# Kernel optimization log

Hardware: AMD Instinct MI355X
Metric: run time of the kernel (lower is better)

## Reference

```python
import jax, jax.numpy as jnp
import numpy as np

B, L0, L1, NS, D, H, NL, HM = 16, 512, 256, 32, 256, 8, 4, 4
T = L0 + L1 + NS + 1
HD = D // H
EPS = 1e-5
SCALE = HD ** -0.5


def setup_inputs() -> dict:
    key = jax.random.key(0)
    ks = jax.random.split(key, 20)
    s = 0.02
    return {
        'seq_tokens_0': jax.random.normal(ks[0], (B, L0, D), jnp.float32),
        'seq_tokens_1': jax.random.normal(ks[1], (B, L1, D), jnp.float32),
        'seq_lens_0': jax.random.randint(ks[2], (B,), 0, L0),
        'seq_lens_1': jax.random.randint(ks[3], (B,), 0, L1),
        'ns_tokens': jax.random.normal(ks[4], (B, NS, D), jnp.float32),
        'domain_emb': jax.random.normal(ks[5], (2, D), jnp.float32) * s,
        'cls_token': jax.random.normal(ks[6], (1, 1, D), jnp.float32) * s,
        'ln1_w': jnp.ones((NL, D), jnp.float32),
        'ln1_b': jnp.zeros((NL, D), jnp.float32),
        'qkv_w': jax.random.normal(ks[7], (NL, D, 3 * D), jnp.float32) * s,
        'qkv_b': jnp.zeros((NL, 3 * D), jnp.float32),
        'out_w': jax.random.normal(ks[8], (NL, D, D), jnp.float32) * s,
        'out_b': jnp.zeros((NL, D), jnp.float32),
        'ln2_w': jnp.ones((NL, D), jnp.float32),
        'ln2_b': jnp.zeros((NL, D), jnp.float32),
        'ffn1_w': jax.random.normal(ks[9], (NL, D, HM * D), jnp.float32) * s,
        'ffn1_b': jnp.zeros((NL, HM * D), jnp.float32),
        'ffn2_w': jax.random.normal(ks[10], (NL, HM * D, D), jnp.float32) * s,
        'ffn2_b': jnp.zeros((NL, D), jnp.float32),
        'fln_w': jnp.ones((D,), jnp.float32),
        'fln_b': jnp.zeros((D,), jnp.float32),
    }


def _ln(x, w, b):
    m = jnp.mean(x, -1, keepdims=True)
    v = jnp.var(x, -1, keepdims=True)
    return (x - m) * jax.lax.rsqrt(v + EPS) * w + b


def _build_mask(seq_lens_0, seq_lens_1):
    # static block structure: intra-domain causal, S<->NS bidirectional, CLS sink row
    base = jnp.zeros((T, T), bool)
    base = base.at[:L0, :L0].set(jnp.tril(jnp.ones((L0, L0), bool)))
    base = base.at[L0:L0 + L1, L0:L0 + L1].set(jnp.tril(jnp.ones((L1, L1), bool)))
    ns_s, ns_e = L0 + L1, L0 + L1 + NS
    base = base.at[:ns_s, ns_s:ns_e].set(True)   # S -> NS
    base = base.at[ns_s:ns_e, :ns_e].set(True)   # NS -> S and NS -> NS
    base = base.at[T - 1, :ns_e].set(True)       # CLS reads all S/NS
    base = base.at[T - 1, T - 1].set(True)       # CLS reads itself
    # per-batch padding mask on keys of each seq segment
    kv = jnp.ones((B, T), bool)
    kv = kv.at[:, :L0].set(jnp.arange(L0)[None, :] < seq_lens_0[:, None])
    kv = kv.at[:, L0:L0 + L1].set(jnp.arange(L1)[None, :] < seq_lens_1[:, None])
    return base[None] & kv[:, None, :]  # [B, T, T]


def _attention(x, mask, qkv_w, qkv_b, out_w, out_b):
    qkv = (x @ qkv_w + qkv_b).reshape(B, T, 3, H, HD)
    q, k, v = qkv[:, :, 0], qkv[:, :, 1], qkv[:, :, 2]
    scores = jnp.einsum('bqhd,bkhd->bhqk', q, k) * SCALE
    m = mask[:, None]  # [B,1,T,T]
    s = jnp.where(m, scores, -jnp.inf)
    any_valid = jnp.any(m, -1, keepdims=True)
    mx = jnp.where(any_valid, jnp.max(s, -1, keepdims=True), 0.0)
    e = jnp.exp(s - mx)  # masked entries exp(-inf)=0
    denom = jnp.sum(e, -1, keepdims=True)
    probs = e / jnp.maximum(denom, 1e-30)  # fully-masked rows -> zeros
    out = jnp.einsum('bhqk,bkhd->bqhd', probs, v).reshape(B, T, D)
    return out @ out_w + out_b


def reference(seq_tokens_0, seq_tokens_1, seq_lens_0, seq_lens_1, ns_tokens,
              domain_emb, cls_token, ln1_w, ln1_b, qkv_w, qkv_b, out_w, out_b,
              ln2_w, ln2_b, ffn1_w, ffn1_b, ffn2_w, ffn2_b, fln_w, fln_b):
    t0 = seq_tokens_0 + domain_emb[0][None, None, :]
    t1 = seq_tokens_1 + domain_emb[1][None, None, :]
    cls = jnp.broadcast_to(cls_token, (B, 1, D))
    x = jnp.concatenate([t0, t1, ns_tokens, cls], axis=1)  # [B,T,D]
    mask = _build_mask(seq_lens_0, seq_lens_1)
    for l in range(NL):
        x = x + _attention(_ln(x, ln1_w[l], ln1_b[l]), mask,
                           qkv_w[l], qkv_b[l], out_w[l], out_b[l])
        h = _ln(x, ln2_w[l], ln2_b[l])
        h = jax.nn.gelu(h @ ffn1_w[l] + ffn1_b[l], approximate=False)
        x = x + h @ ffn2_w[l] + ffn2_b[l]
    x = _ln(x, fln_w, fln_b)
    return x[:, -1, :]  # CLS state [B,D]
```

## Files before the change

kernel.cpp:

```cpp
#include <hip/hip_runtime.h>
#include <hip/hip_bf16.h>
#include <math.h>

typedef __attribute__((ext_vector_type(8))) unsigned short ushort8;
typedef __attribute__((ext_vector_type(8))) short short8;
typedef __attribute__((ext_vector_type(4))) float f32x4;
typedef __attribute__((ext_vector_type(4))) unsigned short ushort4v;
typedef __attribute__((ext_vector_type(4))) int i32x4;
typedef unsigned int u32;

namespace {
constexpr int B = 16, L0 = 512, L1 = 256, NS = 32, D = 256, H = 8, NL = 4, HM = 4;
constexpr int T = L0 + L1 + NS + 1;
constexpr int HD = D / H;
constexpr int NTOK = B * T;
constexpr int NS_S = L0 + L1;
constexpr int NS_E = NS_S + NS;
constexpr int TPAD = 832;
constexpr float EPS = 1e-5f;
constexpr float SCALE = 0.17677669529663687f;
constexpr float SCL2  = 0.17677669529663687f * 1.4426950408889634f;
}

__device__ __forceinline__ ushort f2bf(float f) {
    union { float f; unsigned u; } v; v.f = f;
    return (ushort)((v.u + 0x7fffu + ((v.u >> 16) & 1u)) >> 16);
}

__device__ __forceinline__ u32 cvtpk(float a, float b) {
    u32 r;
    asm("v_cvt_pk_bf16_f32 %0, %1, %2" : "=v"(r) : "v"(a), "v"(b));
    return r;
}

__device__ __forceinline__ void gload_lds16(const void* g, void* l) {
    __builtin_amdgcn_global_load_lds(
        (const __attribute__((address_space(1))) u32*)g,
        (__attribute__((address_space(3))) u32*)l, 16, 0, 0);
}

__global__ __launch_bounds__(256) void k_build_x(
    const float* __restrict__ s0, const float* __restrict__ s1,
    const float* __restrict__ ns, const float* __restrict__ dom,
    const float* __restrict__ cls, float* __restrict__ x)
{
    const int row = blockIdx.x;
    const int b = row / T, t = row % T;
    const int d = threadIdx.x;
    float v;
    if (t < L0)        v = s0[((size_t)b * L0 + t) * D + d] + dom[d];
    else if (t < NS_S) v = s1[((size_t)b * L1 + (t - L0)) * D + d] + dom[D + d];
    else if (t < NS_E) v = ns[((size_t)b * NS + (t - NS_S)) * D + d];
    else               v = cls[d];
    x[(size_t)row * D + d] = v;
}

__global__ __launch_bounds__(256) void k_wprep(
    const float* __restrict__ src, ushort* __restrict__ dst, int K, int N)
{
    const size_t off = (size_t)blockIdx.z * K * N;
    src += off; dst += off;
    __shared__ float t[32][33];
    const int kb = blockIdx.x * 32, nb = blockIdx.y * 32;
    const int c = threadIdx.x & 31, r8 = threadIdx.x >> 5;
#pragma unroll
    for (int rr = 0; rr < 32; rr += 8)
        t[r8 + rr][c] = src[(size_t)(kb + r8 + rr) * N + nb + c];
    __syncthreads();
#pragma unroll
    for (int rr = 0; rr < 32; rr += 8)
        dst[(size_t)(nb + r8 + rr) * K + kb + c] = f2bf(t[c][r8 + rr]);
}

__global__ __launch_bounds__(256) void k_ln(
    const float* __restrict__ x, const float* __restrict__ w,
    const float* __restrict__ bsh, ushort* __restrict__ y, int nrows)
{
    const int wid = threadIdx.x >> 6, lane = threadIdx.x & 63;
    const int row = blockIdx.x * 4 + wid;
    if (row >= nrows) return;
    float4 v = *(const float4*)(x + (size_t)row * D + lane * 4);
    float s  = v.x + v.y + v.z + v.w;
    float ss = v.x * v.x + v.y * v.y + v.z * v.z + v.w * v.w;
#pragma unroll
    for (int o = 32; o; o >>= 1) { s += __shfl_xor(s, o); ss += __shfl_xor(ss, o); }
    const float mean = s * (1.f / D);
    const float var  = ss * (1.f / D) - mean * mean;
    const float r = rsqrtf(var + EPS);
    float4 wv = *(const float4*)(w + lane * 4);
    float4 bv = *(const float4*)(bsh + lane * 4);
    ushort4v o4;
    o4[0] = f2bf((v.x - mean) * r * wv.x + bv.x);
    o4[1] = f2bf((v.y - mean) * r * wv.y + bv.y);
    o4[2] = f2bf((v.z - mean) * r * wv.z + bv.z);
    o4[3] = f2bf((v.w - mean) * r * wv.w + bv.w);
    *(ushort4v*)(y + (size_t)row * D + lane * 4) = o4;
}

__global__ __launch_bounds__(64) void k_final_ln(
    const float* __restrict__ x, const float* __restrict__ w,
    const float* __restrict__ bsh, float* __restrict__ out)
{
    const int b = blockIdx.x, lane = threadIdx.x;
    const float* xr = x + (size_t)(b * T + (T - 1)) * D;
    float4 v = *(const float4*)(xr + lane * 4);
    float s  = v.x + v.y + v.z + v.w;
    float ss = v.x * v.x + v.y * v.y + v.z * v.z + v.w * v.w;
#pragma unroll
    for (int o = 32; o; o >>= 1) { s += __shfl_xor(s, o); ss += __shfl_xor(ss, o); }
    const float mean = s * (1.f / D);
    const float var  = ss * (1.f / D) - mean * mean;
    const float r = rsqrtf(var + EPS);
    float4 wv = *(const float4*)(w + lane * 4);
    float4 bv = *(const float4*)(bsh + lane * 4);
    float4 o4;
    o4.x = (v.x - mean) * r * wv.x + bv.x;
    o4.y = (v.y - mean) * r * wv.y + bv.y;
    o4.z = (v.z - mean) * r * wv.z + bv.z;
    o4.w = (v.w - mean) * r * wv.w + bv.w;
    *(float4*)(out + (size_t)b * D + lane * 4) = o4;
}

template<bool GELU, bool RES, bool OBF>
__global__ __launch_bounds__(256) void k_gemm_mfma(
    const ushort* __restrict__ A, const ushort* __restrict__ Wt,
    const float* __restrict__ bias, void* __restrict__ Cout,
    const float* __restrict__ res, int M, int N, int K)
{
    __shared__ ushort As[2][128 * 64];
    __shared__ ushort Bs[2][128 * 64];
    const int tid = threadIdx.x;
    const int lane = tid & 63, w = tid >> 6;
    const int lo = lane & 15, g = lane >> 4;
    const int wr = w >> 1, wc = w & 1;
    const int m0 = blockIdx.x * 128, n0 = blockIdx.y * 128;

    f32x4 zero = {0.f, 0.f, 0.f, 0.f};
    f32x4 acc[4][4];
#pragma unroll
    for (int mi = 0; mi < 4; ++mi)
#pragma unroll
        for (int ni = 0; ni < 4; ++ni) acc[mi][ni] = zero;

    const ushort* srcA[4];
    const ushort* srcB[4];
    int ldsOff[4];
#pragma unroll
    for (int i = 0; i < 4; ++i) {
        const int idx16 = (w * 4 + i) * 64 + lane;
        const int row = idx16 >> 3;
        const int scb = ((idx16 & 7) * 16) ^ ((row & 7) << 4);
        int arow = m0 + row; if (arow >= M) arow = M - 1;
        srcA[i] = A  + (size_t)arow * K + (scb >> 1);
        srcB[i] = Wt + (size_t)(n0 + row) * K + (scb >> 1);
        ldsOff[i] = (w * 4 + i) * 512;
    }

    const int NT = K >> 6;

#pragma unroll
    for (int i = 0; i < 4; ++i) {
        gload_lds16(srcA[i], &As[0][ldsOff[i]]);
        gload_lds16(srcB[i], &Bs[0][ldsOff[i]]);
    }
    asm volatile("s_waitcnt vmcnt(0)");
    __syncthreads();

    for (int t = 0; t < NT; ++t) {
        const int buf = t & 1;
        if (t + 1 < NT) {
            const int nb = buf ^ 1, ko = (t + 1) * 64;
#pragma unroll
            for (int i = 0; i < 4; ++i) {
                gload_lds16(srcA[i] + ko, &As[nb][ldsOff[i]]);
                gload_lds16(srcB[i] + ko, &Bs[nb][ldsOff[i]]);
            }
        }
#pragma unroll
        for (int kk = 0; kk < 2; ++kk) {
            const int kb = (kk * 64 + g * 16) ^ ((lo & 7) << 4);
            short8 af[4], bfr[4];
#pragma unroll
            for (int mi = 0; mi < 4; ++mi) {
                const int r = wr * 64 + mi * 16 + lo;
                af[mi] = *(const short8*)&As[buf][r * 64 + (kb >> 1)];
            }
#pragma unroll
            for (int ni = 0; ni < 4; ++ni) {
                const int r = wc * 64 + ni * 16 + lo;
                bfr[ni] = *(const short8*)&Bs[buf][r * 64 + (kb >> 1)];
            }
#pragma unroll
            for (int mi = 0; mi < 4; ++mi)
#pragma unroll
                for (int ni = 0; ni < 4; ++ni)
                    acc[mi][ni] = __builtin_amdgcn_mfma_f32_16x16x32_bf16(
                        af[mi], bfr[ni], acc[mi][ni], 0, 0, 0);
        }
        asm volatile("s_waitcnt vmcnt(0)");
        __syncthreads();
    }

    float bv[4];
#pragma unroll
    for (int ni = 0; ni < 4; ++ni) bv[ni] = bias[n0 + wc * 64 + ni * 16 + lo];
#pragma unroll
    for (int mi = 0; mi < 4; ++mi) {
#pragma unroll
        for (int i = 0; i < 4; ++i) {
            const int row = m0 + wr * 64 + mi * 16 + g * 4 + i;
            if (row < M) {
#pragma unroll
                for (int ni = 0; ni < 4; ++ni) {
                    const int col = n0 + wc * 64 + ni * 16 + lo;
                    float v = acc[mi][ni][i] + bv[ni];
                    if (GELU) v = 0.5f * v * (1.0f + erff(v * 0.70710678118654752f));
                    if (RES)  v += res[(size_t)row * N + col];
                    if (OBF) ((ushort*)Cout)[(size_t)row * N + col] = f2bf(v);
                    else     ((float*)Cout)[(size_t)row * N + col] = v;
                }
            }
        }
    }
}

__global__ __launch_bounds__(256) void k_repack(
    const ushort* __restrict__ qkv, ushort* __restrict__ Kb, ushort* __restrict__ Vt)
{
    const int bh = blockIdx.x, tt = blockIdx.y;
    const int b = bh >> 3, h = bh & 7;
    const int tid = threadIdx.x;
    const int r = tid >> 2, c = tid & 3;
    const int t = tt * 64 + r;
    __shared__ ushort vtile[64][40];
    ushort8 k8 = {0,0,0,0,0,0,0,0}, v8 = {0,0,0,0,0,0,0,0};
    if (t < T) {
        const ushort* kp = qkv + ((size_t)(b * T + t) * 3 + 1) * D + h * HD + c * 8;
        k8 = *(const ushort8*)kp;
        v8 = *(const ushort8*)(kp + D);
    }
    *(ushort8*)(Kb + ((size_t)bh * TPAD + tt * 64 + r) * HD + c * 8) = k8;
    *(ushort8*)&vtile[r][c * 8] = v8;
    __syncthreads();
    const int d = tid >> 3, cc = tid & 7;
    ushort8 o;
#pragma unroll
    for (int j = 0; j < 8; ++j) o[j] = vtile[cc * 8 + j][d];
    *(ushort8*)(Vt + ((size_t)bh * HD + d) * TPAD + tt * 64 + cc * 8) = o;
}

__global__ __launch_bounds__(256) void k_flash(
    const ushort* __restrict__ qkv, const ushort* __restrict__ Kb,
    const ushort* __restrict__ Vt, const int* __restrict__ len0,
    const int* __restrict__ len1, ushort* __restrict__ out)
{
    const int bh = blockIdx.x;
    const int qt = 12 - blockIdx.y;
    const int b = bh >> 3, h = bh & 7;
    const int tid = threadIdx.x, lane = tid & 63, w = tid >> 6;
    const int lo = lane & 15, g = lane >> 4;
    const int b4 = g & 1, b5 = g >> 1;
    const int q = qt * 64 + w * 16 + lo;
    const int l0b = len0[b], lim01 = L0 + len1[b];

    int klo = 0, klim;
    if (q < L0)        klim = q;
    else if (q < NS_S) { klo = L0; klim = q; }
    else if (q < NS_E) klim = NS_E - 1;
    else               klim = q;

    int qrow = q; if (qrow > T - 1) qrow = T - 1;
    short8 qf = *(const short8*)(qkv + ((size_t)(b * T + qrow) * 3) * D + h * HD + g * 8);

    const ushort* Kbase = Kb + (size_t)bh * TPAD * HD;
    const ushort* Vbase = Vt + (size_t)bh * HD * TPAD;

    f32x4 acc0 = {0.f, 0.f, 0.f, 0.f}, acc1 = {0.f, 0.f, 0.f, 0.f};
    float mrow = -1e30f, srow = 0.f;

    const int kts = (qt >= 8 && qt < 12) ? 8 : 0;
    const int ntiles = (qt < 12) ? (qt - kts + 2) : 13;
    auto ktile = [&](int it) { int kt = kts + it; return kt > qt ? 12 : kt; };

    short8 kf[4];
    {
        const int k0 = ktile(0) * 64;
#pragma unroll
        for (int n = 0; n < 4; ++n)
            kf[n] = *(const short8*)(Kbase + (size_t)(k0 + n * 16 + lo) * HD + g * 8);
    }

    for (int it = 0; it < ntiles; ++it) {
        const int k0 = ktile(it) * 64;

        const ushort* V0 = Vbase + k0;
        short8 a00 = *(const short8*)(V0 + (size_t)lo * TPAD + g * 8);
        short8 a01 = *(const short8*)(V0 + (size_t)lo * TPAD + 32 + g * 8);
        short8 a10 = *(const short8*)(V0 + (size_t)(16 + lo) * TPAD + g * 8);
        short8 a11 = *(const short8*)(V0 + (size_t)(16 + lo) * TPAD + 32 + g * 8);

        float pv[4][4];
        float tmax = -1e30f;
#pragma unroll
        for (int n = 0; n < 4; ++n) {
            f32x4 z = {0.f, 0.f, 0.f, 0.f};
            f32x4 sn = __builtin_amdgcn_mfma_f32_16x16x32_bf16(kf[n], qf, z, 0, 0, 0);
#pragma unroll
            for (int i = 0; i < 4; ++i) {
                const int k = k0 + n * 16 + g * 4 + i;
                const bool inNS = (k >= NS_S) & (k < NS_E);
                const bool kval = (k < l0b) | ((k >= L0) & (k < lim01)) | (k >= NS_S);
                const bool m = ((k >= klo) & (k <= klim) & kval) | inNS;
                const float sv = m ? sn[i] * SCL2 : -1e30f;
                pv[n][i] = sv;
                tmax = fmaxf(tmax, sv);
            }
        }

        short8 kf2[4];
        if (it + 1 < ntiles) {
            const int k1 = ktile(it + 1) * 64;
#pragma unroll
            for (int n = 0; n < 4; ++n)
                kf2[n] = *(const short8*)(Kbase + (size_t)(k1 + n * 16 + lo) * HD + g * 8);
        }

        tmax = fmaxf(tmax, __shfl_xor(tmax, 16));
        tmax = fmaxf(tmax, __shfl_xor(tmax, 32));
        const float mnew = fmaxf(mrow, tmax);
        const float scl = exp2f(mrow - mnew);
        mrow = mnew;

        u32 C0[4], C1[4];
        float psum = 0.f;
#pragma unroll
        for (int n = 0; n < 4; ++n) {
            float e0 = exp2f(pv[n][0] - mnew);
            float e1 = exp2f(pv[n][1] - mnew);
            float e2 = exp2f(pv[n][2] - mnew);
            float e3 = exp2f(pv[n][3] - mnew);
            psum += (e0 + e1) + (e2 + e3);
            C0[n] = cvtpk(e0, e1);
            C1[n] = cvtpk(e2, e3);
        }
        psum += __shfl_xor(psum, 16);
        psum += __shfl_xor(psum, 32);
        srow = srow * scl + psum;
#pragma unroll
        for (int i = 0; i < 4; ++i) { acc0[i] *= scl; acc1[i] *= scl; }

        u32 pb0u[4], pb1u[4];
#pragma unroll
        for (int n = 0; n < 4; ++n) {
            const u32 F0 = (u32)__shfl_xor((int)C0[n], 16);
            const u32 F1 = (u32)__shfl_xor((int)C1[n], 16);
            const u32 G00 = b4 ? F0 : C0[n];
            const u32 G01 = b4 ? C0[n] : F0;
            const u32 G10 = b4 ? F1 : C1[n];
            const u32 G11 = b4 ? C1[n] : F1;
            const u32 H00 = (u32)__shfl_xor((int)G00, 32);
            const u32 H01 = (u32)__shfl_xor((int)G01, 32);
            const u32 H10 = (u32)__shfl_xor((int)G10, 32);
            const u32 H11 = (u32)__shfl_xor((int)G11, 32);
            const bool keep = (b5 == b4);
            const u32 S00 = keep ? G00 : H00;
            const u32 S01 = keep ? G01 : H01;
            const u32 S10 = keep ? G10 : H10;
            const u32 S11 = keep ? G11 : H11;
            const bool take = (b5 == (n & 1));
            if ((n >> 1) == 0) {
                pb0u[0] = take ? S00 : pb0u[0];
                pb0u[1] = take ? S10 : pb0u[1];
                pb0u[2] = take ? S01 : pb0u[2];
                pb0u[3] = take ? S11 : pb0u[3];
            } else {
                pb1u[0] = take ? S00 : pb1u[0];
                pb1u[1] = take ? S10 : pb1u[1];
                pb1u[2] = take ? S01 : pb1u[2];
                pb1u[3] = take ? S11 : pb1u[3];
            }
        }
        i32x4 t0 = { (int)pb0u[0], (int)pb0u[1], (int)pb0u[2], (int)pb0u[3] };
        i32x4 t1 = { (int)pb1u[0], (int)pb1u[1], (int)pb1u[2], (int)pb1u[3] };
        const short8 pb0 = __builtin_bit_cast(short8, t0);
        const short8 pb1 = __builtin_bit_cast(short8, t1);

        acc0 = __builtin_amdgcn_mfma_f32_16x16x32_bf16(a00, pb0, acc0, 0, 0, 0);
        acc0 = __builtin_amdgcn_mfma_f32_16x16x32_bf16(a01, pb1, acc0, 0, 0, 0);
        acc1 = __builtin_amdgcn_mfma_f32_16x16x32_bf16(a10, pb0, acc1, 0, 0, 0);
        acc1 = __builtin_amdgcn_mfma_f32_16x16x32_bf16(a11, pb1, acc1, 0, 0, 0);

#pragma unroll
        for (int n = 0; n < 4; ++n) kf[n] = kf2[n];
    }

    if (q < T) {
        const float inv = 1.f / fmaxf(srow, 1e-30f);
        ushort* orow = out + (size_t)(b * T + q) * D + h * HD;
        *(u32*)(orow + g * 4)          = cvtpk(acc0[0] * inv, acc0[1] * inv);
        *(u32*)(orow + g * 4 + 2)      = cvtpk(acc0[2] * inv, acc0[3] * inv);
        *(u32*)(orow + 16 + g * 4)     = cvtpk(acc1[0] * inv, acc1[1] * inv);
        *(u32*)(orow + 16 + g * 4 + 2) = cvtpk(acc1[2] * inv, acc1[3] * inv);
    }
}

extern "C" void kernel_launch(void* const* d_in, const int* in_sizes, int n_in,
                              void* d_out, int out_size, void* d_ws, size_t ws_size,
                              hipStream_t stream)
{
    const float* seq0 = (const float*)d_in[0];
    const float* seq1 = (const float*)d_in[1];
    const int*   len0 = (const int*)d_in[2];
    const int*   len1 = (const int*)d_in[3];
    const float* nst  = (const float*)d_in[4];
    const float* dom  = (const float*)d_in[5];
    const float* cls  = (const float*)d_in[6];
    const float* ln1w = (const float*)d_in[7];
    const float* ln1b = (const float*)d_in[8];
    const float* qkvw = (const float*)d_in[9];
    const float* qkvb = (const float*)d_in[10];
    const float* outw = (const float*)d_in[11];
    const float* outb = (const float*)d_in[12];
    const float* ln2w = (const float*)d_in[13];
    const float* ln2b = (const float*)d_in[14];
    const float* f1w  = (const float*)d_in[15];
    const float* f1b  = (const float*)d_in[16];
    const float* f2w  = (const float*)d_in[17];
    const float* f2b  = (const float*)d_in[18];
    const float* flnw = (const float*)d_in[19];
    const float* flnb = (const float*)d_in[20];

    float*  x   = (float*)d_ws;
    ushort* xn  = (ushort*)(x + (size_t)NTOK * D);
    ushort* big = xn + (size_t)NTOK * D;
    ushort* Kb  = big + (size_t)NTOK * HM * D;
    ushort* Vt  = Kb + (size_t)B * H * TPAD * HD;
    ushort* qkvw_t = Vt + (size_t)B * H * TPAD * HD;
    ushort* outw_t = qkvw_t + (size_t)NL * 768 * 256;
    ushort* f1w_t  = outw_t + (size_t)NL * 256 * 256;
    ushort* f2w_t  = f1w_t  + (size_t)NL * 1024 * 256;

    k_wprep<<<dim3(256 / 32, 768 / 32, NL), 256, 0, stream>>>(qkvw, qkvw_t, 256, 768);
    k_wprep<<<dim3(256 / 32, 256 / 32, NL), 256, 0, stream>>>(outw, outw_t, 256, 256);
    k_wprep<<<dim3(256 / 32, 1024 / 32, NL), 256, 0, stream>>>(f1w, f1w_t, 256, 1024);
    k_wprep<<<dim3(1024 / 32, 256 / 32, NL), 256, 0, stream>>>(f2w, f2w_t, 1024, 256);

    k_build_x<<<NTOK, 256, 0, stream>>>(seq0, seq1, nst, dom, cls, x);

    const int lnGrid = (NTOK + 3) / 4;
    const int gmm = (NTOK + 127) / 128;

    for (int l = 0; l < NL; ++l) {
        k_ln<<<lnGrid, 256, 0, stream>>>(x, ln1w + l * D, ln1b + l * D, xn, NTOK);
        k_gemm_mfma<false, false, true><<<dim3(gmm, 6), 256, 0, stream>>>(
            xn, qkvw_t + (size_t)l * 768 * 256, qkvb + (size_t)l * 3 * D, big, nullptr,
            NTOK, 3 * D, D);
        k_repack<<<dim3(B * H, TPAD / 64), 256, 0, stream>>>(big, Kb, Vt);
        k_flash<<<dim3(B * H, TPAD / 64), 256, 0, stream>>>(big, Kb, Vt, len0, len1, xn);
        k_gemm_mfma<false, true, false><<<dim3(gmm, 2), 256, 0, stream>>>(
            xn, outw_t + (size_t)l * 256 * 256, outb + (size_t)l * D, x, x,
            NTOK, D, D);
        k_ln<<<lnGrid, 256, 0, stream>>>(x, ln2w + l * D, ln2b + l * D, xn, NTOK);
        k_gemm_mfma<true, false, true><<<dim3(gmm, 8), 256, 0, stream>>>(
            xn, f1w_t + (size_t)l * 1024 * 256, f1b + (size_t)l * HM * D, big, nullptr,
            NTOK, HM * D, D);
        k_gemm_mfma<false, true, false><<<dim3(gmm, 2), 256, 0, stream>>>(
            big, f2w_t + (size_t)l * 256 * 1024, f2b + (size_t)l * D, x, x,
            NTOK, D, HM * D);
    }
    k_final_ln<<<B, 64, 0, stream>>>(x, flnw, flnb, (float*)d_out);
}
```

Measured before the change: 554.7 us.

## Fuse LayerNorm into residual GEMM epilogues and QKV repack into GEMM output

```diff
diff --git a/kernel.cpp b/kernel.cpp
--- a/kernel.cpp
+++ b/kernel.cpp
@@ -18,7 +18,6 @@
 constexpr int NS_E = NS_S + NS;
 constexpr int TPAD = 832;
 constexpr float EPS = 1e-5f;
-constexpr float SCALE = 0.17677669529663687f;
 constexpr float SCL2  = 0.17677669529663687f * 1.4426950408889634f;
 }
 
@@ -37,22 +36,6 @@
     __builtin_amdgcn_global_load_lds(
         (const __attribute__((address_space(1))) u32*)g,
         (__attribute__((address_space(3))) u32*)l, 16, 0, 0);
-}
-
-__global__ __launch_bounds__(256) void k_build_x(
-    const float* __restrict__ s0, const float* __restrict__ s1,
-    const float* __restrict__ ns, const float* __restrict__ dom,
-    const float* __restrict__ cls, float* __restrict__ x)
-{
-    const int row = blockIdx.x;
-    const int b = row / T, t = row % T;
-    const int d = threadIdx.x;
-    float v;
-    if (t < L0)        v = s0[((size_t)b * L0 + t) * D + d] + dom[d];
-    else if (t < NS_S) v = s1[((size_t)b * L1 + (t - L0)) * D + d] + dom[D + d];
-    else if (t < NS_E) v = ns[((size_t)b * NS + (t - NS_S)) * D + d];
-    else               v = cls[d];
-    x[(size_t)row * D + d] = v;
 }
 
 __global__ __launch_bounds__(256) void k_wprep(
@@ -72,14 +55,32 @@
         dst[(size_t)(nb + r8 + rr) * K + kb + c] = f2bf(t[c][r8 + rr]);
 }
 
-__global__ __launch_bounds__(256) void k_ln(
-    const float* __restrict__ x, const float* __restrict__ w,
-    const float* __restrict__ bsh, ushort* __restrict__ y, int nrows)
+__global__ __launch_bounds__(256) void k_build_ln(
+    const float* __restrict__ s0, const float* __restrict__ s1,
+    const float* __restrict__ ns, const float* __restrict__ dom,
+    const float* __restrict__ cls, const float* __restrict__ lnw,
+    const float* __restrict__ lnb, float* __restrict__ x, ushort* __restrict__ xn)
 {
     const int wid = threadIdx.x >> 6, lane = threadIdx.x & 63;
     const int row = blockIdx.x * 4 + wid;
-    if (row >= nrows) return;
-    float4 v = *(const float4*)(x + (size_t)row * D + lane * 4);
+    if (row >= NTOK) return;
+    const int b = row / T, t = row % T;
+    const int d0 = lane * 4;
+    float4 v;
+    if (t < L0) {
+        v = *(const float4*)(s0 + ((size_t)b * L0 + t) * D + d0);
+        float4 dm = *(const float4*)(dom + d0);
+        v.x += dm.x; v.y += dm.y; v.z += dm.z; v.w += dm.w;
+    } else if (t < NS_S) {
+        v = *(const float4*)(s1 + ((size_t)b * L1 + (t - L0)) * D + d0);
+        float4 dm = *(const float4*)(dom + D + d0);
+        v.x += dm.x; v.y += dm.y; v.z += dm.z; v.w += dm.w;
+    } else if (t < NS_E) {
+        v = *(const float4*)(ns + ((size_t)b * NS + (t - NS_S)) * D + d0);
+    } else {
+        v = *(const float4*)(cls + d0);
+    }
+    *(float4*)(x + (size_t)row * D + d0) = v;
     float s  = v.x + v.y + v.z + v.w;
     float ss = v.x * v.x + v.y * v.y + v.z * v.z + v.w * v.w;
 #pragma unroll
@@ -87,45 +88,20 @@
     const float mean = s * (1.f / D);
     const float var  = ss * (1.f / D) - mean * mean;
     const float r = rsqrtf(var + EPS);
-    float4 wv = *(const float4*)(w + lane * 4);
-    float4 bv = *(const float4*)(bsh + lane * 4);
+    float4 wv = *(const float4*)(lnw + d0);
+    float4 bv = *(const float4*)(lnb + d0);
     ushort4v o4;
     o4[0] = f2bf((v.x - mean) * r * wv.x + bv.x);
     o4[1] = f2bf((v.y - mean) * r * wv.y + bv.y);
     o4[2] = f2bf((v.z - mean) * r * wv.z + bv.z);
     o4[3] = f2bf((v.w - mean) * r * wv.w + bv.w);
-    *(ushort4v*)(y + (size_t)row * D + lane * 4) = o4;
-}
-
-__global__ __launch_bounds__(64) void k_final_ln(
-    const float* __restrict__ x, const float* __restrict__ w,
-    const float* __restrict__ bsh, float* __restrict__ out)
-{
-    const int b = blockIdx.x, lane = threadIdx.x;
-    const float* xr = x + (size_t)(b * T + (T - 1)) * D;
-    float4 v = *(const float4*)(xr + lane * 4);
-    float s  = v.x + v.y + v.z + v.w;
-    float ss = v.x * v.x + v.y * v.y + v.z * v.z + v.w * v.w;
-#pragma unroll
-    for (int o = 32; o; o >>= 1) { s += __shfl_xor(s, o); ss += __shfl_xor(ss, o); }
-    const float mean = s * (1.f / D);
-    const float var  = ss * (1.f / D) - mean * mean;
-    const float r = rsqrtf(var + EPS);
-    float4 wv = *(const float4*)(w + lane * 4);
-    float4 bv = *(const float4*)(bsh + lane * 4);
-    float4 o4;
-    o4.x = (v.x - mean) * r * wv.x + bv.x;
-    o4.y = (v.y - mean) * r * wv.y + bv.y;
-    o4.z = (v.z - mean) * r * wv.z + bv.z;
-    o4.w = (v.w - mean) * r * wv.w + bv.w;
-    *(float4*)(out + (size_t)b * D + lane * 4) = o4;
-}
-
-template<bool GELU, bool RES, bool OBF>
-__global__ __launch_bounds__(256) void k_gemm_mfma(
+    *(ushort4v*)(xn + (size_t)row * D + d0) = o4;
+}
+
+__global__ __launch_bounds__(256) void k_gemm_qkv(
     const ushort* __restrict__ A, const ushort* __restrict__ Wt,
-    const float* __restrict__ bias, void* __restrict__ Cout,
-    const float* __restrict__ res, int M, int N, int K)
+    const float* __restrict__ bias, ushort* __restrict__ Qo,
+    ushort* __restrict__ Kb, ushort* __restrict__ Vt, int M, int K)
 {
     __shared__ ushort As[2][128 * 64];
     __shared__ ushort Bs[2][128 * 64];
@@ -157,7 +133,6 @@
     }
 
     const int NT = K >> 6;
-
 #pragma unroll
     for (int i = 0; i < 4; ++i) {
         gload_lds16(srcA[i], &As[0][ldsOff[i]]);
@@ -181,15 +156,11 @@
             const int kb = (kk * 64 + g * 16) ^ ((lo & 7) << 4);
             short8 af[4], bfr[4];
 #pragma unroll
-            for (int mi = 0; mi < 4; ++mi) {
-                const int r = wr * 64 + mi * 16 + lo;
-                af[mi] = *(const short8*)&As[buf][r * 64 + (kb >> 1)];
-            }
-#pragma unroll
-            for (int ni = 0; ni < 4; ++ni) {
-                const int r = wc * 64 + ni * 16 + lo;
-                bfr[ni] = *(const short8*)&Bs[buf][r * 64 + (kb >> 1)];
-            }
+            for (int mi = 0; mi < 4; ++mi)
+                af[mi] = *(const short8*)&As[buf][(wr * 64 + mi * 16 + lo) * 64 + (kb >> 1)];
+#pragma unroll
+            for (int ni = 0; ni < 4; ++ni)
+                bfr[ni] = *(const short8*)&Bs[buf][(wc * 64 + ni * 16 + lo) * 64 + (kb >> 1)];
 #pragma unroll
             for (int mi = 0; mi < 4; ++mi)
 #pragma unroll
@@ -201,56 +172,270 @@
         __syncthreads();
     }
 
+    const int cb = n0 + wc * 64;
     float bv[4];
 #pragma unroll
-    for (int ni = 0; ni < 4; ++ni) bv[ni] = bias[n0 + wc * 64 + ni * 16 + lo];
+    for (int ni = 0; ni < 4; ++ni) bv[ni] = bias[cb + ni * 16 + lo];
 #pragma unroll
     for (int mi = 0; mi < 4; ++mi) {
 #pragma unroll
         for (int i = 0; i < 4; ++i) {
             const int row = m0 + wr * 64 + mi * 16 + g * 4 + i;
+            if (row >= M) continue;
+            const int bq = row / T;
+            const int tq = row - bq * T;
+#pragma unroll
+            for (int ni = 0; ni < 4; ++ni) {
+                const int col = cb + ni * 16 + lo;
+                const ushort h16 = f2bf(acc[mi][ni][i] + bv[ni]);
+                if (col < 256) {
+                    Qo[(size_t)row * 256 + col] = h16;
+                } else if (col < 512) {
+                    const int c = col - 256;
+                    Kb[((size_t)(bq * 8 + (c >> 5)) * TPAD + tq) * HD + (c & 31)] = h16;
+                } else {
+                    const int c = col - 512;
+                    Vt[((size_t)(bq * 8 + (c >> 5)) * HD + (c & 31)) * TPAD + tq] = h16;
+                }
+            }
+        }
+    }
+}
+
+__global__ __launch_bounds__(256) void k_gemm_ffn1(
+    const ushort* __restrict__ A, const ushort* __restrict__ Wt,
+    const float* __restrict__ bias, ushort* __restrict__ Cout, int M, int N, int K)
+{
+    __shared__ ushort As[2][128 * 64];
+    __shared__ ushort Bs[2][128 * 64];
+    const int tid = threadIdx.x;
+    const int lane = tid & 63, w = tid >> 6;
+    const int lo = lane & 15, g = lane >> 4;
+    const int wr = w >> 1, wc = w & 1;
+    const int m0 = blockIdx.x * 128, n0 = blockIdx.y * 128;
+
+    f32x4 zero = {0.f, 0.f, 0.f, 0.f};
+    f32x4 acc[4][4];
+#pragma unroll
+    for (int mi = 0; mi < 4; ++mi)
+#pragma unroll
+        for (int ni = 0; ni < 4; ++ni) acc[mi][ni] = zero;
+
+    const ushort* srcA[4];
+    const ushort* srcB[4];
+    int ldsOff[4];
+#pragma unroll
+    for (int i = 0; i < 4; ++i) {
+        const int idx16 = (w * 4 + i) * 64 + lane;
+        const int row = idx16 >> 3;
+        const int scb = ((idx16 & 7) * 16) ^ ((row & 7) << 4);
+        int arow = m0 + row; if (arow >= M) arow = M - 1;
+        srcA[i] = A  + (size_t)arow * K + (scb >> 1);
+        srcB[i] = Wt + (size_t)(n0 + row) * K + (scb >> 1);
+        ldsOff[i] = (w * 4 + i) * 512;
+    }
+
+    const int NT = K >> 6;
+#pragma unroll
+    for (int i = 0; i < 4; ++i) {
+        gload_lds16(srcA[i], &As[0][ldsOff[i]]);
+        gload_lds16(srcB[i], &Bs[0][ldsOff[i]]);
+    }
+    asm volatile("s_waitcnt vmcnt(0)");
+    __syncthreads();
+
+    for (int t = 0; t < NT; ++t) {
+        const int buf = t & 1;
+        if (t + 1 < NT) {
+            const int nb = buf ^ 1, ko = (t + 1) * 64;
+#pragma unroll
+            for (int i = 0; i < 4; ++i) {
+                gload_lds16(srcA[i] + ko, &As[nb][ldsOff[i]]);
+                gload_lds16(srcB[i] + ko, &Bs[nb][ldsOff[i]]);
+            }
+        }
+#pragma unroll
+        for (int kk = 0; kk < 2; ++kk) {
+            const int kb = (kk * 64 + g * 16) ^ ((lo & 7) << 4);
+            short8 af[4], bfr[4];
+#pragma unroll
+            for (int mi = 0; mi < 4; ++mi)
+                af[mi] = *(const short8*)&As[buf][(wr * 64 + mi * 16 + lo) * 64 + (kb >> 1)];
+#pragma unroll
+            for (int ni = 0; ni < 4; ++ni)
+                bfr[ni] = *(const short8*)&Bs[buf][(wc * 64 + ni * 16 + lo) * 64 + (kb >> 1)];
+#pragma unroll
+            for (int mi = 0; mi < 4; ++mi)
+#pragma unroll
+                for (int ni = 0; ni < 4; ++ni)
+                    acc[mi][ni] = __builtin_amdgcn_mfma_f32_16x16x32_bf16(
+                        af[mi], bfr[ni], acc[mi][ni], 0, 0, 0);
+        }
+        asm volatile("s_waitcnt vmcnt(0)");
+        __syncthreads();
+    }
+
+    float bv[4];
+#pragma unroll
+    for (int ni = 0; ni < 4; ++ni) bv[ni] = bias[n0 + wc * 64 + ni * 16 + lo];
+#pragma unroll
+    for (int mi = 0; mi < 4; ++mi) {
+#pragma unroll
+        for (int i = 0; i < 4; ++i) {
+            const int row = m0 + wr * 64 + mi * 16 + g * 4 + i;
+            if (row >= M) continue;
+#pragma unroll
+            for (int ni = 0; ni < 4; ++ni) {
+                const int col = n0 + wc * 64 + ni * 16 + lo;
+                float v = acc[mi][ni][i] + bv[ni];
+                v = 0.5f * v * (1.0f + erff(v * 0.70710678118654752f));
+                Cout[(size_t)row * N + col] = f2bf(v);
+            }
+        }
+    }
+}
+
+template<int MODE>
+__global__ __launch_bounds__(256) void k_gemm_fused(
+    const ushort* __restrict__ A, const ushort* __restrict__ Wt,
+    const float* __restrict__ bias, const float* __restrict__ res,
+    const float* __restrict__ lnw, const float* __restrict__ lnb,
+    float* __restrict__ xout, ushort* __restrict__ xnout,
+    float* __restrict__ dout, int M, int K)
+{
+    __shared__ ushort As[64 * 64];
+    __shared__ ushort Bs[256 * 64];
+    __shared__ float redS[64][4];
+    __shared__ float redQ[64][4];
+    const int tid = threadIdx.x;
+    const int lane = tid & 63, w = tid >> 6;
+    const int lo = lane & 15, g = lane >> 4;
+    const int m0 = blockIdx.x * 64;
+
+    f32x4 zero = {0.f, 0.f, 0.f, 0.f};
+    f32x4 acc[4][4];
+#pragma unroll
+    for (int mi = 0; mi < 4; ++mi)
+#pragma unroll
+        for (int ni = 0; ni < 4; ++ni) acc[mi][ni] = zero;
+
+    const ushort* srcA[2]; int ldsOffA[2];
+    const ushort* srcB[8]; int ldsOffB[8];
+#pragma unroll
+    for (int j = 0; j < 2; ++j) {
+        const int idx16 = j * 256 + tid;
+        const int row = idx16 >> 3;
+        const int scb = ((idx16 & 7) * 16) ^ ((row & 7) << 4);
+        int arow = m0 + row; if (arow >= M) arow = M - 1;
+        srcA[j] = A + (size_t)arow * K + (scb >> 1);
+        ldsOffA[j] = idx16 * 8;
+    }
+#pragma unroll
+    for (int j = 0; j < 8; ++j) {
+        const int idx16 = j * 256 + tid;
+        const int row = idx16 >> 3;
+        const int scb = ((idx16 & 7) * 16) ^ ((row & 7) << 4);
+        srcB[j] = Wt + (size_t)row * K + (scb >> 1);
+        ldsOffB[j] = idx16 * 8;
+    }
+
+    const int NT = K >> 6;
+    for (int t = 0; t < NT; ++t) {
+        const int ko = t * 64;
+        __syncthreads();
+#pragma unroll
+        for (int j = 0; j < 2; ++j) gload_lds16(srcA[j] + ko, &As[ldsOffA[j]]);
+#pragma unroll
+        for (int j = 0; j < 8; ++j) gload_lds16(srcB[j] + ko, &Bs[ldsOffB[j]]);
+        asm volatile("s_waitcnt vmcnt(0)");
+        __syncthreads();
+#pragma unroll
+        for (int kk = 0; kk < 2; ++kk) {
+            const int kb = (kk * 64 + g * 16) ^ ((lo & 7) << 4);
+            short8 af[4], bfr[4];
+#pragma unroll
+            for (int mi = 0; mi < 4; ++mi)
+                af[mi] = *(const short8*)&As[(mi * 16 + lo) * 64 + (kb >> 1)];
+#pragma unroll
+            for (int ni = 0; ni < 4; ++ni)
+                bfr[ni] = *(const short8*)&Bs[(w * 64 + ni * 16 + lo) * 64 + (kb >> 1)];
+#pragma unroll
+            for (int mi = 0; mi < 4; ++mi)
+#pragma unroll
+                for (int ni = 0; ni < 4; ++ni)
+                    acc[mi][ni] = __builtin_amdgcn_mfma_f32_16x16x32_bf16(
+                        af[mi], bfr[ni], acc[mi][ni], 0, 0, 0);
+        }
+    }
+
+    float bv[4], lw[4], lb[4];
+#pragma unroll
+    for (int ni = 0; ni < 4; ++ni) {
+        const int c = w * 64 + ni * 16 + lo;
+        bv[ni] = bias[c]; lw[ni] = lnw[c]; lb[ni] = lnb[c];
+    }
+#pragma unroll
+    for (int mi = 0; mi < 4; ++mi) {
+#pragma unroll
+        for (int i = 0; i < 4; ++i) {
+            const int r64 = mi * 16 + g * 4 + i;
+            const int row = m0 + r64;
+            float s = 0.f, q = 0.f;
             if (row < M) {
 #pragma unroll
                 for (int ni = 0; ni < 4; ++ni) {
-                    const int col = n0 + wc * 64 + ni * 16 + lo;
-                    float v = acc[mi][ni][i] + bv[ni];
-                    if (GELU) v = 0.5f * v * (1.0f + erff(v * 0.70710678118654752f));
-                    if (RES)  v += res[(size_t)row * N + col];
-                    if (OBF) ((ushort*)Cout)[(size_t)row * N + col] = f2bf(v);
-                    else     ((float*)Cout)[(size_t)row * N + col] = v;
+                    const int col = w * 64 + ni * 16 + lo;
+                    float v = acc[mi][ni][i] + bv[ni] + res[(size_t)row * 256 + col];
+                    acc[mi][ni][i] = v;
+                    s += v; q += v * v;
                 }
-            }
-        }
-    }
-}
-
-__global__ __launch_bounds__(256) void k_repack(
-    const ushort* __restrict__ qkv, ushort* __restrict__ Kb, ushort* __restrict__ Vt)
-{
-    const int bh = blockIdx.x, tt = blockIdx.y;
-    const int b = bh >> 3, h = bh & 7;
-    const int tid = threadIdx.x;
-    const int r = tid >> 2, c = tid & 3;
-    const int t = tt * 64 + r;
-    __shared__ ushort vtile[64][40];
-    ushort8 k8 = {0,0,0,0,0,0,0,0}, v8 = {0,0,0,0,0,0,0,0};
-    if (t < T) {
-        const ushort* kp = qkv + ((size_t)(b * T + t) * 3 + 1) * D + h * HD + c * 8;
-        k8 = *(const ushort8*)kp;
-        v8 = *(const ushort8*)(kp + D);
-    }
-    *(ushort8*)(Kb + ((size_t)bh * TPAD + tt * 64 + r) * HD + c * 8) = k8;
-    *(ushort8*)&vtile[r][c * 8] = v8;
+                s += __shfl_xor(s, 1); q += __shfl_xor(q, 1);
+                s += __shfl_xor(s, 2); q += __shfl_xor(q, 2);
+                s += __shfl_xor(s, 4); q += __shfl_xor(q, 4);
+                s += __shfl_xor(s, 8); q += __shfl_xor(q, 8);
+                if (lo == 0) { redS[r64][w] = s; redQ[r64][w] = q; }
+            }
+        }
+    }
     __syncthreads();
-    const int d = tid >> 3, cc = tid & 7;
-    ushort8 o;
-#pragma unroll
-    for (int j = 0; j < 8; ++j) o[j] = vtile[cc * 8 + j][d];
-    *(ushort8*)(Vt + ((size_t)bh * HD + d) * TPAD + tt * 64 + cc * 8) = o;
+#pragma unroll
+    for (int mi = 0; mi < 4; ++mi) {
+#pragma unroll
+        for (int i = 0; i < 4; ++i) {
+            const int r64 = mi * 16 + g * 4 + i;
+            const int row = m0 + r64;
+            if (row >= M) continue;
+            const float S = redS[r64][0] + redS[r64][1] + redS[r64][2] + redS[r64][3];
+            const float Q = redQ[r64][0] + redQ[r64][1] + redQ[r64][2] + redQ[r64][3];
+            const float mean = S * (1.f / 256.f);
+            const float var  = Q * (1.f / 256.f) - mean * mean;
+            const float rstd = rsqrtf(var + EPS);
+            if (MODE == 0) {
+#pragma unroll
+                for (int ni = 0; ni < 4; ++ni) {
+                    const int col = w * 64 + ni * 16 + lo;
+                    const float v = acc[mi][ni][i];
+                    xout[(size_t)row * 256 + col] = v;
+                    xnout[(size_t)row * 256 + col] = f2bf((v - mean) * rstd * lw[ni] + lb[ni]);
+                }
+            } else {
+                const int bq = row / T;
+                const int tq = row - bq * T;
+                if (tq == T - 1) {
+#pragma unroll
+                    for (int ni = 0; ni < 4; ++ni) {
+                        const int col = w * 64 + ni * 16 + lo;
+                        dout[(size_t)bq * 256 + col] =
+                            (acc[mi][ni][i] - mean) * rstd * lw[ni] + lb[ni];
+                    }
+                }
+            }
+        }
+    }
 }
 
 __global__ __launch_bounds__(256) void k_flash(
-    const ushort* __restrict__ qkv, const ushort* __restrict__ Kb,
+    const ushort* __restrict__ Qo, const ushort* __restrict__ Kb,
     const ushort* __restrict__ Vt, const int* __restrict__ len0,
     const int* __restrict__ len1, ushort* __restrict__ out)
 {
@@ -270,7 +455,7 @@
     else               klim = q;
 
     int qrow = q; if (qrow > T - 1) qrow = T - 1;
-    short8 qf = *(const short8*)(qkv + ((size_t)(b * T + qrow) * 3) * D + h * HD + g * 8);
+    short8 qf = *(const short8*)(Qo + (size_t)(b * T + qrow) * D + h * HD + g * 8);
 
     const ushort* Kbase = Kb + (size_t)bh * TPAD * HD;
     const ushort* Vbase = Vt + (size_t)bh * HD * TPAD;
@@ -445,28 +630,31 @@
     k_wprep<<<dim3(256 / 32, 1024 / 32, NL), 256, 0, stream>>>(f1w, f1w_t, 256, 1024);
     k_wprep<<<dim3(1024 / 32, 256 / 32, NL), 256, 0, stream>>>(f2w, f2w_t, 1024, 256);
 
-    k_build_x<<<NTOK, 256, 0, stream>>>(seq0, seq1, nst, dom, cls, x);
-
-    const int lnGrid = (NTOK + 3) / 4;
+    k_build_ln<<<(NTOK + 3) / 4, 256, 0, stream>>>(seq0, seq1, nst, dom, cls,
+                                                   ln1w, ln1b, x, xn);
+
     const int gmm = (NTOK + 127) / 128;
+    const int gf  = (NTOK + 63) / 64;
 
     for (int l = 0; l < NL; ++l) {
-        k_ln<<<lnGrid, 256, 0, stream>>>(x, ln1w + l * D, ln1b + l * D, xn, NTOK);
-        k_gemm_mfma<false, false, true><<<dim3(gmm, 6), 256, 0, stream>>>(
-            xn, qkvw_t + (size_t)l * 768 * 256, qkvb + (size_t)l * 3 * D, big, nullptr,
-            NTOK, 3 * D, D);
-        k_repack<<<dim3(B * H, TPAD / 64), 256, 0, stream>>>(big, Kb, Vt);
+        k_gemm_qkv<<<dim3(gmm, 6), 256, 0, stream>>>(
+            xn, qkvw_t + (size_t)l * 768 * 256, qkvb + (size_t)l * 3 * D,
+            big, Kb, Vt, NTOK, D);
         k_flash<<<dim3(B * H, TPAD / 64), 256, 0, stream>>>(big, Kb, Vt, len0, len1, xn);
-        k_gemm_mfma<false, true, false><<<dim3(gmm, 2), 256, 0, stream>>>(
-            xn, outw_t + (size_t)l * 256 * 256, outb + (size_t)l * D, x, x,
-            NTOK, D, D);
-        k_ln<<<lnGrid, 256, 0, stream>>>(x, ln2w + l * D, ln2b + l * D, xn, NTOK);
-        k_gemm_mfma<true, false, true><<<dim3(gmm, 8), 256, 0, stream>>>(
-            xn, f1w_t + (size_t)l * 1024 * 256, f1b + (size_t)l * HM * D, big, nullptr,
+        k_gemm_fused<0><<<gf, 256, 0, stream>>>(
+            xn, outw_t + (size_t)l * 256 * 256, outb + (size_t)l * D, x,
+            ln2w + l * D, ln2b + l * D, x, xn, nullptr, NTOK, D);
+        k_gemm_ffn1<<<dim3(gmm, 8), 256, 0, stream>>>(
+            xn, f1w_t + (size_t)l * 1024 * 256, f1b + (size_t)l * HM * D, big,
             NTOK, HM * D, D);
-        k_gemm_mfma<false, true, false><<<dim3(gmm, 2), 256, 0, stream>>>(
-            big, f2w_t + (size_t)l * 256 * 1024, f2b + (size_t)l * D, x, x,
-            NTOK, D, HM * D);
-    }
-    k_final_ln<<<B, 64, 0, stream>>>(x, flnw, flnb, (float*)d_out);
-}
+        if (l < NL - 1) {
+            k_gemm_fused<0><<<gf, 256, 0, stream>>>(
+                big, f2w_t + (size_t)l * 256 * 1024, f2b + (size_t)l * D, x,
+                ln1w + (l + 1) * D, ln1b + (l + 1) * D, x, xn, nullptr, NTOK, HM * D);
+        } else {
+            k_gemm_fused<1><<<gf, 256, 0, stream>>>(
+                big, f2w_t + (size_t)l * 256 * 1024, f2b + (size_t)l * D, x,
+                flnw, flnb, nullptr, nullptr, (float*)d_out, NTOK, HM * D);
+        }
+    }
+}
```

New measurement: 608.0 us. 1.1x slower.
